# Kernel tuning notes

Hardware: AMD Instinct MI355X
Metric: run time of the kernel (lower is better)

The kernel has to match this reference:

```python
import jax, jax.numpy as jnp
import numpy as np

B, N, D_POINTS, D_MODEL = 2, 65536, 64, 128
SCALE = 1.0 / np.float32(np.sqrt(D_MODEL))


def setup_inputs() -> dict:
    key = jax.random.key(0)
    ks = jax.random.split(key, 20)
    def lin(k, fan_in, fan_out):
        s = 1.0 / np.sqrt(fan_in)
        return jax.random.uniform(k, (fan_in, fan_out), jnp.float32, -s, s)
    return {
        "xyz": jax.random.normal(ks[0], (B, N, 3), jnp.float32),
        "features": jax.random.normal(ks[1], (B, N, D_POINTS), jnp.float32),
        "fc1_w": lin(ks[2], D_POINTS, D_MODEL), "fc1_b": jnp.zeros((D_MODEL,), jnp.float32),
        "fc2_w": lin(ks[3], D_MODEL, D_POINTS), "fc2_b": jnp.zeros((D_POINTS,), jnp.float32),
        "d1_w": lin(ks[4], 3, D_MODEL), "d1_b": jnp.zeros((D_MODEL,), jnp.float32),
        "d2_w": lin(ks[5], D_MODEL, D_MODEL), "d2_b": jnp.zeros((D_MODEL,), jnp.float32),
        "g1_w": lin(ks[6], D_MODEL, D_MODEL), "g1_b": jnp.zeros((D_MODEL,), jnp.float32),
        "g2_w": lin(ks[7], D_MODEL, D_MODEL), "g2_b": jnp.zeros((D_MODEL,), jnp.float32),
        "wq": lin(ks[8], D_MODEL, D_MODEL),
        "wk": lin(ks[9], D_MODEL, D_MODEL),
        "wv": lin(ks[10], D_MODEL, D_MODEL),
    }


def reference(xyz, features, fc1_w, fc1_b, fc2_w, fc2_b, d1_w, d1_b, d2_w, d2_b,
              g1_w, g1_b, g2_w, g2_b, wq, wk, wv):
    # x: [B, N, d_model]
    x = features @ fc1_w + fc1_b
    q = x @ wq
    k = x @ wk
    v = x @ wv
    # position encoding MLP on xyz: [B, N, d_model]
    pos_enc = jax.nn.relu(xyz @ d1_w + d1_b) @ d2_w + d2_b
    # vector attention: elementwise q - k + pos_enc, gamma MLP, per-channel softmax over points
    attn = jax.nn.relu((q - k + pos_enc) @ g1_w + g1_b) @ g2_w + g2_b
    attn = jax.nn.softmax(attn * SCALE, axis=-2)  # softmax over N (point axis)
    # elementwise gating of values
    res = attn * (v + pos_enc)
    res = res @ fc2_w + fc2_b + features  # residual
    return (res, attn)
```

## Files before the change

kernel.cpp:

```cpp
#include <hip/hip_runtime.h>
#include <hip/hip_bf16.h>

#define BB 2
#define NN 65536
#define DP 64
#define DM 128
#define SCALEF 0.08838834764831845f

typedef __attribute__((ext_vector_type(8))) short short8v;
typedef __attribute__((ext_vector_type(4))) float float4v;

__device__ __forceinline__ unsigned fenc(float f) {
  unsigned u = __float_as_uint(f);
  return (u & 0x80000000u) ? ~u : (u | 0x80000000u);
}
__device__ __forceinline__ float fdec(unsigned u) {
  unsigned v = (u & 0x80000000u) ? (u & 0x7FFFFFFFu) : ~u;
  return __uint_as_float(v);
}
__device__ __forceinline__ unsigned short f2bf(float f) {
  unsigned u = __float_as_uint(f);
  u += 0x7FFFu + ((u >> 16) & 1u);
  return (unsigned short)(u >> 16);
}
__device__ __forceinline__ float bf2f(unsigned short h) {
  return __uint_as_float(((unsigned)h) << 16);
}

__global__ __launch_bounds__(256) void k0_kernel(
    const float* __restrict__ wq, const float* __restrict__ wk,
    const float* __restrict__ fc1_w, const float* __restrict__ d2_w,
    const float* __restrict__ g1_w, const float* __restrict__ g2_w,
    const float* __restrict__ wv_w,
    float* __restrict__ zbuf,
    short* __restrict__ d2t, short* __restrict__ fc1t, short* __restrict__ wqkt,
    short* __restrict__ g1t, short* __restrict__ g2t, short* __restrict__ wvt) {
  int t = threadIdx.x, bi = blockIdx.x;
  if (bi < 2) zbuf[bi * 256 + t] = 0.f;
  int mat = bi >> 5, blk = bi & 31;
  if (mat == 1) {
    int i = blk * 256 + t;
    int n = i >> 6, k = i & 63;
    fc1t[n * 64 + k] = (short)f2bf(fc1_w[k * 128 + n]);
  } else {
    const float* src = (mat == 0) ? d2_w : (mat == 2) ? wq : (mat == 3) ? g1_w
                     : (mat == 4) ? g2_w : wv_w;
    short* dst = (mat == 0) ? d2t : (mat == 2) ? wqkt : (mat == 3) ? g1t
               : (mat == 4) ? g2t : wvt;
#pragma unroll
    for (int j = 0; j < 2; ++j) {
      int i = blk * 512 + t + j * 256;
      int n = i >> 7, k = i & 127;
      float v = src[k * 128 + n];
      if (mat == 2) v -= wk[k * 128 + n];
      dst[n * 128 + k] = (short)f2bf(v);
    }
  }
}

template<int K>
__device__ __forceinline__ void gemm_mfma(const short* __restrict__ A,
                                          const short* __restrict__ Wt,
                                          short* __restrict__ Ws,
                                          int tid, int wv, int col, int quad,
                                          float4v acc[4][2]) {
#pragma unroll
  for (int h = 0; h < K / 64; ++h) {
    __syncthreads();
#pragma unroll
    for (int j = 0; j < 4; ++j) {
      int i = tid + j * 256;
      int row = i >> 3, kc = (i & 7) * 8;
      *(short8v*)(Ws + row * 72 + kc) = *(const short8v*)(Wt + row * K + h * 64 + kc);
    }
    __syncthreads();
#pragma unroll
    for (int ks = 0; ks < 2; ++ks) {
      int ko = h * 64 + ks * 32 + quad * 8;
      int wo = ks * 32 + quad * 8;
      short8v b0 = *(const short8v*)(Ws + (wv * 32 + col) * 72 + wo);
      short8v b1 = *(const short8v*)(Ws + (wv * 32 + 16 + col) * 72 + wo);
#pragma unroll
      for (int mt = 0; mt < 4; ++mt) {
        short8v a = *(const short8v*)(A + (mt * 16 + col) * 136 + ko);
        acc[mt][0] = __builtin_amdgcn_mfma_f32_16x16x32_bf16(a, b0, acc[mt][0], 0, 0, 0);
        acc[mt][1] = __builtin_amdgcn_mfma_f32_16x16x32_bf16(a, b1, acc[mt][1], 0, 0, 0);
      }
    }
  }
}

__device__ __forceinline__ void store_tile(short* __restrict__ dst,
                                           const float4v acc[4][2],
                                           int wv, int col, int quad,
                                           float b0, float b1, bool do_relu) {
#pragma unroll
  for (int mt = 0; mt < 4; ++mt)
#pragma unroll
    for (int nt = 0; nt < 2; ++nt) {
      float bias = nt ? b1 : b0;
#pragma unroll
      for (int r = 0; r < 4; ++r) {
        float v = acc[mt][nt][r] + bias;
        if (do_relu) v = fmaxf(v, 0.f);
        dst[(mt * 16 + quad * 4 + r) * 136 + wv * 32 + nt * 16 + col] = (short)f2bf(v);
      }
    }
}

__global__ __launch_bounds__(256, 2) void k1_kernel(
    const float* __restrict__ xyz, const float* __restrict__ features,
    const short* __restrict__ fc1t, const float* __restrict__ fc1_b,
    const float* __restrict__ d1_w, const float* __restrict__ d1_b,
    const short* __restrict__ d2t, const float* __restrict__ d2_b,
    const short* __restrict__ g1t, const float* __restrict__ g1_b,
    const short* __restrict__ g2t, const float* __restrict__ g2_b,
    const short* __restrict__ wqkt, const short* __restrict__ wvt,
    float* __restrict__ out_logits, unsigned short* __restrict__ Gbf,
    unsigned* __restrict__ maxenc) {
  __shared__ short As[64 * 136];
  __shared__ short Xs[64 * 136];
  __shared__ short Ws[128 * 72];

  const int tid = threadIdx.x;
  const int wv = tid >> 6;
  const int lane = tid & 63;
  const int col = lane & 15, quad = lane >> 4;
  const long long p0 = (long long)blockIdx.x * 64;
  const int b = (int)(p0 >> 16);

  float* xf = (float*)Xs;
  if (tid < 192) xf[tid] = xyz[p0 * 3 + tid];
  __syncthreads();

  {
    const int tn = tid & 31, tm = tid >> 5;
    const int c4 = tn * 4, pbase = tm * 8;
    float4 w0 = *(const float4*)(d1_w + c4);
    float4 w1 = *(const float4*)(d1_w + 128 + c4);
    float4 w2 = *(const float4*)(d1_w + 256 + c4);
    float4 bb = *(const float4*)(d1_b + c4);
#pragma unroll
    for (int p = 0; p < 8; ++p) {
      float x0 = xf[(pbase + p) * 3 + 0];
      float x1 = xf[(pbase + p) * 3 + 1];
      float x2 = xf[(pbase + p) * 3 + 2];
      short4 rr;
      rr.x = (short)f2bf(fmaxf(0.f, fmaf(x0, w0.x, fmaf(x1, w1.x, fmaf(x2, w2.x, bb.x)))));
      rr.y = (short)f2bf(fmaxf(0.f, fmaf(x0, w0.y, fmaf(x1, w1.y, fmaf(x2, w2.y, bb.y)))));
      rr.z = (short)f2bf(fmaxf(0.f, fmaf(x0, w0.z, fmaf(x1, w1.z, fmaf(x2, w2.z, bb.z)))));
      rr.w = (short)f2bf(fmaxf(0.f, fmaf(x0, w0.w, fmaf(x1, w1.w, fmaf(x2, w2.w, bb.w)))));
      *(short4*)(As + (pbase + p) * 136 + c4) = rr;
    }
  }

  const int ch0 = wv * 32 + col, ch1 = ch0 + 16;
  float4v pe[4][2], acc[4][2];

#pragma unroll
  for (int mt = 0; mt < 4; ++mt)
#pragma unroll
    for (int nt = 0; nt < 2; ++nt)
#pragma unroll
      for (int r = 0; r < 4; ++r) acc[mt][nt][r] = 0.f;
  gemm_mfma<128>(As, d2t, Ws, tid, wv, col, quad, acc);
  {
    float b0 = d2_b[ch0], b1 = d2_b[ch1];
#pragma unroll
    for (int mt = 0; mt < 4; ++mt)
#pragma unroll
      for (int r = 0; r < 4; ++r) {
        pe[mt][0][r] = acc[mt][0][r] + b0;
        pe[mt][1][r] = acc[mt][1][r] + b1;
      }
  }
  __syncthreads();

#pragma unroll
  for (int j = 0; j < 4; ++j) {
    int c = tid + j * 256;
    float4 f = *(const float4*)(features + p0 * 64 + (long long)c * 4);
    int row = c >> 4, cp = (c & 15) * 4;
    short4 s;
    s.x = (short)f2bf(f.x); s.y = (short)f2bf(f.y);
    s.z = (short)f2bf(f.z); s.w = (short)f2bf(f.w);
    *(short4*)(As + row * 136 + cp) = s;
  }
#pragma unroll
  for (int mt = 0; mt < 4; ++mt)
#pragma unroll
    for (int nt = 0; nt < 2; ++nt)
#pragma unroll
      for (int r = 0; r < 4; ++r) acc[mt][nt][r] = 0.f;
  gemm_mfma<64>(As, fc1t, Ws, tid, wv, col, quad, acc);
  store_tile(Xs, acc, wv, col, quad, fc1_b[ch0], fc1_b[ch1], false);

#pragma unroll
  for (int mt = 0; mt < 4; ++mt)
#pragma unroll
    for (int nt = 0; nt < 2; ++nt)
#pragma unroll
      for (int r = 0; r < 4; ++r) acc[mt][nt][r] = pe[mt][nt][r];
  gemm_mfma<128>(Xs, wqkt, Ws, tid, wv, col, quad, acc);
  store_tile(As, acc, wv, col, quad, 0.f, 0.f, false);

#pragma unroll
  for (int mt = 0; mt < 4; ++mt)
#pragma unroll
    for (int nt = 0; nt < 2; ++nt)
#pragma unroll
      for (int r = 0; r < 4; ++r) acc[mt][nt][r] = 0.f;
  gemm_mfma<128>(As, g1t, Ws, tid, wv, col, quad, acc);
  __syncthreads();
  store_tile(As, acc, wv, col, quad, g1_b[ch0], g1_b[ch1], true);

#pragma unroll
  for (int mt = 0; mt < 4; ++mt)
#pragma unroll
    for (int nt = 0; nt < 2; ++nt)
#pragma unroll
      for (int r = 0; r < 4; ++r) acc[mt][nt][r] = 0.f;
  gemm_mfma<128>(As, g2t, Ws, tid, wv, col, quad, acc);
  {
    float b0 = g2_b[ch0], b1 = g2_b[ch1];
    float mx0 = -3.4e38f, mx1 = -3.4e38f;
#pragma unroll
    for (int mt = 0; mt < 4; ++mt)
#pragma unroll
      for (int r = 0; r < 4; ++r) {
        long long row = p0 + mt * 16 + quad * 4 + r;
        float v0 = acc[mt][0][r] + b0;
        float v1 = acc[mt][1][r] + b1;
        out_logits[row * DM + ch0] = v0;
        out_logits[row * DM + ch1] = v1;
        mx0 = fmaxf(mx0, v0); mx1 = fmaxf(mx1, v1);
      }
    mx0 = fmaxf(mx0, __shfl_xor(mx0, 16, 64));
    mx0 = fmaxf(mx0, __shfl_xor(mx0, 32, 64));
    mx1 = fmaxf(mx1, __shfl_xor(mx1, 16, 64));
    mx1 = fmaxf(mx1, __shfl_xor(mx1, 32, 64));
    if (quad == 0) {
      atomicMax(&maxenc[b * DM + ch0], fenc(mx0));
      atomicMax(&maxenc[b * DM + ch1], fenc(mx1));
    }
  }

#pragma unroll
  for (int mt = 0; mt < 4; ++mt)
#pragma unroll
    for (int nt = 0; nt < 2; ++nt)
#pragma unroll
      for (int r = 0; r < 4; ++r) acc[mt][nt][r] = pe[mt][nt][r];
  gemm_mfma<128>(Xs, wvt, Ws, tid, wv, col, quad, acc);
#pragma unroll
  for (int mt = 0; mt < 4; ++mt)
#pragma unroll
    for (int r = 0; r < 4; ++r) {
      long long row = p0 + mt * 16 + quad * 4 + r;
      Gbf[row * DM + ch0] = f2bf(acc[mt][0][r]);
      Gbf[row * DM + ch1] = f2bf(acc[mt][1][r]);
    }
}

__global__ __launch_bounds__(256) void k2_kernel(const float* __restrict__ logits,
                                                 const unsigned* __restrict__ maxenc,
                                                 float* __restrict__ sums) {
  __shared__ float red[8 * DM];
  const int tid = threadIdx.x;
  const int c4 = (tid & 31) * 4, r = tid >> 5;
  const long long pb = (long long)blockIdx.x * 256;
  const int b = (int)(pb >> 16);
  float4 m;
  m.x = fdec(maxenc[b * DM + c4 + 0]); m.y = fdec(maxenc[b * DM + c4 + 1]);
  m.z = fdec(maxenc[b * DM + c4 + 2]); m.w = fdec(maxenc[b * DM + c4 + 3]);
  float4 s = {0.f, 0.f, 0.f, 0.f};
  for (int i = 0; i < 32; ++i) {
    long long p = pb + r + (long long)i * 8;
    float4 l = *(const float4*)(logits + p * DM + c4);
    s.x += __expf((l.x - m.x) * SCALEF);
    s.y += __expf((l.y - m.y) * SCALEF);
    s.z += __expf((l.z - m.z) * SCALEF);
    s.w += __expf((l.w - m.w) * SCALEF);
  }
  *(float4*)(red + r * DM + c4) = s;
  __syncthreads();
  if (tid < DM) {
    float t = 0.f;
#pragma unroll
    for (int rr = 0; rr < 8; ++rr) t += red[rr * DM + tid];
    atomicAdd(&sums[b * DM + tid], t);
  }
}

__global__ __launch_bounds__(256) void k3_kernel(
    float* __restrict__ attn_io,
    float* __restrict__ out_res,
    const unsigned short* __restrict__ Gbf,
    const float* __restrict__ sums, const unsigned* __restrict__ maxenc,
    const float* __restrict__ fc2_w, const float* __restrict__ fc2_b,
    const float* __restrict__ features) {
  __shared__ float Ys[64 * DM];
  __shared__ float W2[DM * DP];
  const int tid = threadIdx.x;
#pragma unroll
  for (int j = 0; j < 8; ++j)
    ((float4*)W2)[tid + j * 256] = ((const float4*)fc2_w)[tid + j * 256];

  const long long p0 = (long long)blockIdx.x * 64;
  const int b = (int)(p0 >> 16);
  const int tn = tid & 31, tm = tid >> 5;
  const int c4 = tn * 4, pbase = tm * 8;

  float4 m, sv;
  m.x = fdec(maxenc[b * DM + c4 + 0]); m.y = fdec(maxenc[b * DM + c4 + 1]);
  m.z = fdec(maxenc[b * DM + c4 + 2]); m.w = fdec(maxenc[b * DM + c4 + 3]);
  sv.x = 1.f / sums[b * DM + c4 + 0]; sv.y = 1.f / sums[b * DM + c4 + 1];
  sv.z = 1.f / sums[b * DM + c4 + 2]; sv.w = 1.f / sums[b * DM + c4 + 3];

#pragma unroll
  for (int p = 0; p < 8; ++p) {
    long long idx = (p0 + pbase + p) * DM + c4;
    float4 l = *(const float4*)(attn_io + idx);
    float4 a;
    a.x = __expf((l.x - m.x) * SCALEF) * sv.x;
    a.y = __expf((l.y - m.y) * SCALEF) * sv.y;
    a.z = __expf((l.z - m.z) * SCALEF) * sv.z;
    a.w = __expf((l.w - m.w) * SCALEF) * sv.w;
    *(float4*)(attn_io + idx) = a;
    ushort4 g = *(const ushort4*)(Gbf + idx);
    float4 y;
    y.x = a.x * bf2f(g.x); y.y = a.y * bf2f(g.y);
    y.z = a.z * bf2f(g.z); y.w = a.w * bf2f(g.w);
    *(float4*)(Ys + (pbase + p) * DM + c4) = y;
  }
  __syncthreads();

  const int tn2 = tid & 15, tm2 = tid >> 4;
  const int c4b = tn2 * 4, pb2 = tm2 * 4;
  float acc[4][4];
#pragma unroll
  for (int p = 0; p < 4; ++p)
    acc[p][0] = acc[p][1] = acc[p][2] = acc[p][3] = 0.f;

  for (int k = 0; k < DM; k += 4) {
    float4 a4[4];
#pragma unroll
    for (int p = 0; p < 4; ++p)
      a4[p] = *(const float4*)(Ys + (pb2 + p) * DM + k);
#pragma unroll
    for (int i = 0; i < 4; ++i) {
      float4 w4 = *(const float4*)(W2 + (k + i) * DP + c4b);
#pragma unroll
      for (int p = 0; p < 4; ++p) {
        float a = (i == 0) ? a4[p].x : (i == 1) ? a4[p].y : (i == 2) ? a4[p].z : a4[p].w;
        acc[p][0] = fmaf(a, w4.x, acc[p][0]);
        acc[p][1] = fmaf(a, w4.y, acc[p][1]);
        acc[p][2] = fmaf(a, w4.z, acc[p][2]);
        acc[p][3] = fmaf(a, w4.w, acc[p][3]);
      }
    }
  }
  float4 bb = *(const float4*)(fc2_b + c4b);
#pragma unroll
  for (int p = 0; p < 4; ++p) {
    float4 ft = *(const float4*)(features + (p0 + pb2 + p) * DP + c4b);
    float4 o;
    o.x = acc[p][0] + bb.x + ft.x; o.y = acc[p][1] + bb.y + ft.y;
    o.z = acc[p][2] + bb.z + ft.z; o.w = acc[p][3] + bb.w + ft.w;
    *(float4*)(out_res + (p0 + pb2 + p) * DP + c4b) = o;
  }
}

extern "C" void kernel_launch(void* const* d_in, const int* in_sizes, int n_in,
                              void* d_out, int out_size, void* d_ws, size_t ws_size,
                              hipStream_t stream) {
  const float* xyz      = (const float*)d_in[0];
  const float* features = (const float*)d_in[1];
  const float* fc1_w    = (const float*)d_in[2];
  const float* fc1_b    = (const float*)d_in[3];
  const float* fc2_w    = (const float*)d_in[4];
  const float* fc2_b    = (const float*)d_in[5];
  const float* d1_w     = (const float*)d_in[6];
  const float* d1_b     = (const float*)d_in[7];
  const float* d2_w     = (const float*)d_in[8];
  const float* d2_b     = (const float*)d_in[9];
  const float* g1_w     = (const float*)d_in[10];
  const float* g1_b     = (const float*)d_in[11];
  const float* g2_w     = (const float*)d_in[12];
  const float* g2_b     = (const float*)d_in[13];
  const float* wq       = (const float*)d_in[14];
  const float* wk       = (const float*)d_in[15];
  const float* wv       = (const float*)d_in[16];

  float* out_res  = (float*)d_out;
  float* out_attn = out_res + (long long)BB * NN * DP;

  float*    sums   = (float*)d_ws;
  unsigned* maxenc = (unsigned*)d_ws + 256;
  short* wbase = (short*)((float*)d_ws + 512);
  short* d2t  = wbase;
  short* fc1t = d2t + 16384;
  short* wqkt = fc1t + 8192;
  short* g1t  = wqkt + 16384;
  short* g2t  = g1t + 16384;
  short* wvt  = g2t + 16384;
  unsigned short* Gbf = (unsigned short*)d_out;

  hipLaunchKernelGGL(k0_kernel, dim3(192), dim3(256), 0, stream,
                     wq, wk, fc1_w, d2_w, g1_w, g2_w, wv,
                     (float*)d_ws, d2t, fc1t, wqkt, g1t, g2t, wvt);
  hipLaunchKernelGGL(k1_kernel, dim3((BB * NN) / 64), dim3(256), 0, stream,
                     xyz, features, fc1t, fc1_b, d1_w, d1_b, d2t, d2_b,
                     g1t, g1_b, g2t, g2_b, wqkt, wvt, out_attn, Gbf, maxenc);
  hipLaunchKernelGGL(k2_kernel, dim3((BB * NN) / 256), dim3(256), 0, stream,
                     out_attn, maxenc, sums);
  hipLaunchKernelGGL(k3_kernel, dim3((BB * NN) / 64), dim3(256), 0, stream,
                     out_attn, out_res, Gbf, sums, maxenc, fc2_w, fc2_b, features);
}
```

Measured before the change: 281.2 us.

## Drop max pass, fuse exp/sum into k1, MFMA fc2, register-resident weights

Removes the separate max-reduction and sum kernel. k1 now computes exp of the scaled logits directly, stores them as bf16 and atomically accumulates per-channel sums, so the softmax max subtraction is skipped. Weight tiles are loaded straight into registers instead of staged through shared memory, and occupancy is raised to three blocks. The final fc2 projection moves to bf16 MFMA with a pre-transposed weight. The risks are overflow without max subtraction if logits grow large, and extra bf16 rounding of the exponentials and of the gated values.

Result: faster. 237.1 us (-15.7%).

```diff
diff --git a/kernel.cpp b/kernel.cpp
--- a/kernel.cpp
+++ b/kernel.cpp
@@ -10,14 +10,6 @@
 typedef __attribute__((ext_vector_type(8))) short short8v;
 typedef __attribute__((ext_vector_type(4))) float float4v;
 
-__device__ __forceinline__ unsigned fenc(float f) {
-  unsigned u = __float_as_uint(f);
-  return (u & 0x80000000u) ? ~u : (u | 0x80000000u);
-}
-__device__ __forceinline__ float fdec(unsigned u) {
-  unsigned v = (u & 0x80000000u) ? (u & 0x7FFFFFFFu) : ~u;
-  return __uint_as_float(v);
-}
 __device__ __forceinline__ unsigned short f2bf(float f) {
   unsigned u = __float_as_uint(f);
   u += 0x7FFFu + ((u >> 16) & 1u);
@@ -29,19 +21,24 @@
 
 __global__ __launch_bounds__(256) void k0_kernel(
     const float* __restrict__ wq, const float* __restrict__ wk,
-    const float* __restrict__ fc1_w, const float* __restrict__ d2_w,
-    const float* __restrict__ g1_w, const float* __restrict__ g2_w,
-    const float* __restrict__ wv_w,
-    float* __restrict__ zbuf,
+    const float* __restrict__ fc1_w, const float* __restrict__ fc2_w,
+    const float* __restrict__ d2_w, const float* __restrict__ g1_w,
+    const float* __restrict__ g2_w, const float* __restrict__ wv_w,
+    float* __restrict__ sums,
     short* __restrict__ d2t, short* __restrict__ fc1t, short* __restrict__ wqkt,
-    short* __restrict__ g1t, short* __restrict__ g2t, short* __restrict__ wvt) {
+    short* __restrict__ g1t, short* __restrict__ g2t, short* __restrict__ wvt,
+    short* __restrict__ fc2t) {
   int t = threadIdx.x, bi = blockIdx.x;
-  if (bi < 2) zbuf[bi * 256 + t] = 0.f;
+  if (bi == 0) sums[t] = 0.f;
   int mat = bi >> 5, blk = bi & 31;
   if (mat == 1) {
     int i = blk * 256 + t;
     int n = i >> 6, k = i & 63;
     fc1t[n * 64 + k] = (short)f2bf(fc1_w[k * 128 + n]);
+  } else if (mat == 6) {
+    int i = blk * 256 + t;
+    int n = i >> 7, k = i & 127;
+    fc2t[n * 128 + k] = (short)f2bf(fc2_w[k * 64 + n]);
   } else {
     const float* src = (mat == 0) ? d2_w : (mat == 2) ? wq : (mat == 3) ? g1_w
                      : (mat == 4) ? g2_w : wv_w;
@@ -59,40 +56,33 @@
 }
 
 template<int K>
-__device__ __forceinline__ void gemm_mfma(const short* __restrict__ A,
-                                          const short* __restrict__ Wt,
-                                          short* __restrict__ Ws,
-                                          int tid, int wv, int col, int quad,
-                                          float4v acc[4][2]) {
-#pragma unroll
-  for (int h = 0; h < K / 64; ++h) {
-    __syncthreads();
-#pragma unroll
-    for (int j = 0; j < 4; ++j) {
-      int i = tid + j * 256;
-      int row = i >> 3, kc = (i & 7) * 8;
-      *(short8v*)(Ws + row * 72 + kc) = *(const short8v*)(Wt + row * K + h * 64 + kc);
-    }
-    __syncthreads();
-#pragma unroll
-    for (int ks = 0; ks < 2; ++ks) {
-      int ko = h * 64 + ks * 32 + quad * 8;
-      int wo = ks * 32 + quad * 8;
-      short8v b0 = *(const short8v*)(Ws + (wv * 32 + col) * 72 + wo);
-      short8v b1 = *(const short8v*)(Ws + (wv * 32 + 16 + col) * 72 + wo);
-#pragma unroll
-      for (int mt = 0; mt < 4; ++mt) {
-        short8v a = *(const short8v*)(A + (mt * 16 + col) * 136 + ko);
-        acc[mt][0] = __builtin_amdgcn_mfma_f32_16x16x32_bf16(a, b0, acc[mt][0], 0, 0, 0);
-        acc[mt][1] = __builtin_amdgcn_mfma_f32_16x16x32_bf16(a, b1, acc[mt][1], 0, 0, 0);
-      }
+__device__ __forceinline__ void loadB(const short* __restrict__ Wt,
+                                      int wid, int col, int quad, short8v b[2][4]) {
+#pragma unroll
+  for (int nt = 0; nt < 2; ++nt)
+#pragma unroll
+    for (int kt = 0; kt < K / 32; ++kt)
+      b[nt][kt] = *(const short8v*)(Wt + (wid * 32 + nt * 16 + col) * K + kt * 32 + quad * 8);
+}
+
+template<int K>
+__device__ __forceinline__ void gemm_compute(const short* __restrict__ A,
+                                             const short8v b[2][4],
+                                             int col, int quad, float4v acc[4][2]) {
+#pragma unroll
+  for (int kt = 0; kt < K / 32; ++kt) {
+#pragma unroll
+    for (int mt = 0; mt < 4; ++mt) {
+      short8v a = *(const short8v*)(A + (mt * 16 + col) * 136 + kt * 32 + quad * 8);
+      acc[mt][0] = __builtin_amdgcn_mfma_f32_16x16x32_bf16(a, b[0][kt], acc[mt][0], 0, 0, 0);
+      acc[mt][1] = __builtin_amdgcn_mfma_f32_16x16x32_bf16(a, b[1][kt], acc[mt][1], 0, 0, 0);
     }
   }
 }
 
 __device__ __forceinline__ void store_tile(short* __restrict__ dst,
                                            const float4v acc[4][2],
-                                           int wv, int col, int quad,
+                                           int wid, int col, int quad,
                                            float b0, float b1, bool do_relu) {
 #pragma unroll
   for (int mt = 0; mt < 4; ++mt)
@@ -103,12 +93,17 @@
       for (int r = 0; r < 4; ++r) {
         float v = acc[mt][nt][r] + bias;
         if (do_relu) v = fmaxf(v, 0.f);
-        dst[(mt * 16 + quad * 4 + r) * 136 + wv * 32 + nt * 16 + col] = (short)f2bf(v);
+        dst[(mt * 16 + quad * 4 + r) * 136 + wid * 32 + nt * 16 + col] = (short)f2bf(v);
       }
     }
 }
 
-__global__ __launch_bounds__(256, 2) void k1_kernel(
+#define ZERO_ACC(acc) \
+  _Pragma("unroll") for (int mt = 0; mt < 4; ++mt) \
+  _Pragma("unroll") for (int nt = 0; nt < 2; ++nt) \
+  _Pragma("unroll") for (int r = 0; r < 4; ++r) acc[mt][nt][r] = 0.f;
+
+__global__ __launch_bounds__(256, 3) void k1_kernel(
     const float* __restrict__ xyz, const float* __restrict__ features,
     const short* __restrict__ fc1t, const float* __restrict__ fc1_b,
     const float* __restrict__ d1_w, const float* __restrict__ d1_b,
@@ -116,18 +111,19 @@
     const short* __restrict__ g1t, const float* __restrict__ g1_b,
     const short* __restrict__ g2t, const float* __restrict__ g2_b,
     const short* __restrict__ wqkt, const short* __restrict__ wvt,
-    float* __restrict__ out_logits, unsigned short* __restrict__ Gbf,
-    unsigned* __restrict__ maxenc) {
-  __shared__ short As[64 * 136];
-  __shared__ short Xs[64 * 136];
-  __shared__ short Ws[128 * 72];
+    unsigned short* __restrict__ Ebf, unsigned short* __restrict__ Gbf,
+    float* __restrict__ sums) {
+  __shared__ __align__(16) short As[64 * 136];
+  __shared__ __align__(16) short Xs[64 * 136];
 
   const int tid = threadIdx.x;
-  const int wv = tid >> 6;
-  const int lane = tid & 63;
+  const int wid = tid >> 6, lane = tid & 63;
   const int col = lane & 15, quad = lane >> 4;
   const long long p0 = (long long)blockIdx.x * 64;
-  const int b = (int)(p0 >> 16);
+  const int bi = (int)(p0 >> 16);
+
+  short8v b[2][4];
+  loadB<128>(d2t, wid, col, quad, b);
 
   float* xf = (float*)Xs;
   if (tid < 192) xf[tid] = xyz[p0 * 3 + tid];
@@ -153,17 +149,13 @@
       *(short4*)(As + (pbase + p) * 136 + c4) = rr;
     }
   }
-
-  const int ch0 = wv * 32 + col, ch1 = ch0 + 16;
+  __syncthreads();
+
+  const int ch0 = wid * 32 + col, ch1 = ch0 + 16;
   float4v pe[4][2], acc[4][2];
 
-#pragma unroll
-  for (int mt = 0; mt < 4; ++mt)
-#pragma unroll
-    for (int nt = 0; nt < 2; ++nt)
-#pragma unroll
-      for (int r = 0; r < 4; ++r) acc[mt][nt][r] = 0.f;
-  gemm_mfma<128>(As, d2t, Ws, tid, wv, col, quad, acc);
+  ZERO_ACC(acc)
+  gemm_compute<128>(As, b, col, quad, acc);
   {
     float b0 = d2_b[ch0], b1 = d2_b[ch1];
 #pragma unroll
@@ -174,6 +166,7 @@
         pe[mt][1][r] = acc[mt][1][r] + b1;
       }
   }
+  loadB<64>(fc1t, wid, col, quad, b);
   __syncthreads();
 
 #pragma unroll
@@ -186,72 +179,64 @@
     s.z = (short)f2bf(f.z); s.w = (short)f2bf(f.w);
     *(short4*)(As + row * 136 + cp) = s;
   }
+  __syncthreads();
+
+  ZERO_ACC(acc)
+  gemm_compute<64>(As, b, col, quad, acc);
+  store_tile(Xs, acc, wid, col, quad, fc1_b[ch0], fc1_b[ch1], false);
+  loadB<128>(wqkt, wid, col, quad, b);
+  __syncthreads();
+
 #pragma unroll
   for (int mt = 0; mt < 4; ++mt)
 #pragma unroll
     for (int nt = 0; nt < 2; ++nt)
 #pragma unroll
-      for (int r = 0; r < 4; ++r) acc[mt][nt][r] = 0.f;
-  gemm_mfma<64>(As, fc1t, Ws, tid, wv, col, quad, acc);
-  store_tile(Xs, acc, wv, col, quad, fc1_b[ch0], fc1_b[ch1], false);
-
-#pragma unroll
-  for (int mt = 0; mt < 4; ++mt)
-#pragma unroll
-    for (int nt = 0; nt < 2; ++nt)
-#pragma unroll
       for (int r = 0; r < 4; ++r) acc[mt][nt][r] = pe[mt][nt][r];
-  gemm_mfma<128>(Xs, wqkt, Ws, tid, wv, col, quad, acc);
-  store_tile(As, acc, wv, col, quad, 0.f, 0.f, false);
-
-#pragma unroll
-  for (int mt = 0; mt < 4; ++mt)
-#pragma unroll
-    for (int nt = 0; nt < 2; ++nt)
-#pragma unroll
-      for (int r = 0; r < 4; ++r) acc[mt][nt][r] = 0.f;
-  gemm_mfma<128>(As, g1t, Ws, tid, wv, col, quad, acc);
-  __syncthreads();
-  store_tile(As, acc, wv, col, quad, g1_b[ch0], g1_b[ch1], true);
-
-#pragma unroll
-  for (int mt = 0; mt < 4; ++mt)
-#pragma unroll
-    for (int nt = 0; nt < 2; ++nt)
-#pragma unroll
-      for (int r = 0; r < 4; ++r) acc[mt][nt][r] = 0.f;
-  gemm_mfma<128>(As, g2t, Ws, tid, wv, col, quad, acc);
+  gemm_compute<128>(Xs, b, col, quad, acc);
+  store_tile(As, acc, wid, col, quad, 0.f, 0.f, false);
+  loadB<128>(g1t, wid, col, quad, b);
+  __syncthreads();
+
+  ZERO_ACC(acc)
+  gemm_compute<128>(As, b, col, quad, acc);
+  __syncthreads();
+  store_tile(As, acc, wid, col, quad, g1_b[ch0], g1_b[ch1], true);
+  loadB<128>(g2t, wid, col, quad, b);
+  __syncthreads();
+
+  ZERO_ACC(acc)
+  gemm_compute<128>(As, b, col, quad, acc);
   {
     float b0 = g2_b[ch0], b1 = g2_b[ch1];
-    float mx0 = -3.4e38f, mx1 = -3.4e38f;
+    float s0 = 0.f, s1 = 0.f;
 #pragma unroll
     for (int mt = 0; mt < 4; ++mt)
 #pragma unroll
       for (int r = 0; r < 4; ++r) {
         long long row = p0 + mt * 16 + quad * 4 + r;
-        float v0 = acc[mt][0][r] + b0;
-        float v1 = acc[mt][1][r] + b1;
-        out_logits[row * DM + ch0] = v0;
-        out_logits[row * DM + ch1] = v1;
-        mx0 = fmaxf(mx0, v0); mx1 = fmaxf(mx1, v1);
+        float e0 = __expf((acc[mt][0][r] + b0) * SCALEF);
+        float e1 = __expf((acc[mt][1][r] + b1) * SCALEF);
+        Ebf[row * DM + ch0] = f2bf(e0);
+        Ebf[row * DM + ch1] = f2bf(e1);
+        s0 += e0; s1 += e1;
       }
-    mx0 = fmaxf(mx0, __shfl_xor(mx0, 16, 64));
-    mx0 = fmaxf(mx0, __shfl_xor(mx0, 32, 64));
-    mx1 = fmaxf(mx1, __shfl_xor(mx1, 16, 64));
-    mx1 = fmaxf(mx1, __shfl_xor(mx1, 32, 64));
+    s0 += __shfl_xor(s0, 16, 64); s0 += __shfl_xor(s0, 32, 64);
+    s1 += __shfl_xor(s1, 16, 64); s1 += __shfl_xor(s1, 32, 64);
     if (quad == 0) {
-      atomicMax(&maxenc[b * DM + ch0], fenc(mx0));
-      atomicMax(&maxenc[b * DM + ch1], fenc(mx1));
-    }
-  }
-
+      atomicAdd(&sums[bi * DM + ch0], s0);
+      atomicAdd(&sums[bi * DM + ch1], s1);
+    }
+  }
+
+  loadB<128>(wvt, wid, col, quad, b);
 #pragma unroll
   for (int mt = 0; mt < 4; ++mt)
 #pragma unroll
     for (int nt = 0; nt < 2; ++nt)
 #pragma unroll
       for (int r = 0; r < 4; ++r) acc[mt][nt][r] = pe[mt][nt][r];
-  gemm_mfma<128>(Xs, wvt, Ws, tid, wv, col, quad, acc);
+  gemm_compute<128>(Xs, b, col, quad, acc);
 #pragma unroll
   for (int mt = 0; mt < 4; ++mt)
 #pragma unroll
@@ -262,113 +247,69 @@
     }
 }
 
-__global__ __launch_bounds__(256) void k2_kernel(const float* __restrict__ logits,
-                                                 const unsigned* __restrict__ maxenc,
-                                                 float* __restrict__ sums) {
-  __shared__ float red[8 * DM];
+__global__ __launch_bounds__(256) void k3_kernel(
+    const unsigned short* __restrict__ Ebf, float* __restrict__ out_attn,
+    float* __restrict__ out_res, const unsigned short* __restrict__ Gbf,
+    const float* __restrict__ sums,
+    const short* __restrict__ fc2t, const float* __restrict__ fc2_b,
+    const float* __restrict__ features) {
+  __shared__ __align__(16) short Ys[64 * 136];
   const int tid = threadIdx.x;
-  const int c4 = (tid & 31) * 4, r = tid >> 5;
-  const long long pb = (long long)blockIdx.x * 256;
-  const int b = (int)(pb >> 16);
-  float4 m;
-  m.x = fdec(maxenc[b * DM + c4 + 0]); m.y = fdec(maxenc[b * DM + c4 + 1]);
-  m.z = fdec(maxenc[b * DM + c4 + 2]); m.w = fdec(maxenc[b * DM + c4 + 3]);
-  float4 s = {0.f, 0.f, 0.f, 0.f};
-  for (int i = 0; i < 32; ++i) {
-    long long p = pb + r + (long long)i * 8;
-    float4 l = *(const float4*)(logits + p * DM + c4);
-    s.x += __expf((l.x - m.x) * SCALEF);
-    s.y += __expf((l.y - m.y) * SCALEF);
-    s.z += __expf((l.z - m.z) * SCALEF);
-    s.w += __expf((l.w - m.w) * SCALEF);
-  }
-  *(float4*)(red + r * DM + c4) = s;
-  __syncthreads();
-  if (tid < DM) {
-    float t = 0.f;
-#pragma unroll
-    for (int rr = 0; rr < 8; ++rr) t += red[rr * DM + tid];
-    atomicAdd(&sums[b * DM + tid], t);
-  }
-}
-
-__global__ __launch_bounds__(256) void k3_kernel(
-    float* __restrict__ attn_io,
-    float* __restrict__ out_res,
-    const unsigned short* __restrict__ Gbf,
-    const float* __restrict__ sums, const unsigned* __restrict__ maxenc,
-    const float* __restrict__ fc2_w, const float* __restrict__ fc2_b,
-    const float* __restrict__ features) {
-  __shared__ float Ys[64 * DM];
-  __shared__ float W2[DM * DP];
-  const int tid = threadIdx.x;
-#pragma unroll
-  for (int j = 0; j < 8; ++j)
-    ((float4*)W2)[tid + j * 256] = ((const float4*)fc2_w)[tid + j * 256];
-
   const long long p0 = (long long)blockIdx.x * 64;
-  const int b = (int)(p0 >> 16);
-  const int tn = tid & 31, tm = tid >> 5;
-  const int c4 = tn * 4, pbase = tm * 8;
-
-  float4 m, sv;
-  m.x = fdec(maxenc[b * DM + c4 + 0]); m.y = fdec(maxenc[b * DM + c4 + 1]);
-  m.z = fdec(maxenc[b * DM + c4 + 2]); m.w = fdec(maxenc[b * DM + c4 + 3]);
-  sv.x = 1.f / sums[b * DM + c4 + 0]; sv.y = 1.f / sums[b * DM + c4 + 1];
-  sv.z = 1.f / sums[b * DM + c4 + 2]; sv.w = 1.f / sums[b * DM + c4 + 3];
-
-#pragma unroll
-  for (int p = 0; p < 8; ++p) {
-    long long idx = (p0 + pbase + p) * DM + c4;
-    float4 l = *(const float4*)(attn_io + idx);
-    float4 a;
-    a.x = __expf((l.x - m.x) * SCALEF) * sv.x;
-    a.y = __expf((l.y - m.y) * SCALEF) * sv.y;
-    a.z = __expf((l.z - m.z) * SCALEF) * sv.z;
-    a.w = __expf((l.w - m.w) * SCALEF) * sv.w;
-    *(float4*)(attn_io + idx) = a;
-    ushort4 g = *(const ushort4*)(Gbf + idx);
-    float4 y;
-    y.x = a.x * bf2f(g.x); y.y = a.y * bf2f(g.y);
-    y.z = a.z * bf2f(g.z); y.w = a.w * bf2f(g.w);
-    *(float4*)(Ys + (pbase + p) * DM + c4) = y;
-  }
-  __syncthreads();
-
-  const int tn2 = tid & 15, tm2 = tid >> 4;
-  const int c4b = tn2 * 4, pb2 = tm2 * 4;
-  float acc[4][4];
-#pragma unroll
-  for (int p = 0; p < 4; ++p)
-    acc[p][0] = acc[p][1] = acc[p][2] = acc[p][3] = 0.f;
-
-  for (int k = 0; k < DM; k += 4) {
-    float4 a4[4];
-#pragma unroll
-    for (int p = 0; p < 4; ++p)
-      a4[p] = *(const float4*)(Ys + (pb2 + p) * DM + k);
-#pragma unroll
-    for (int i = 0; i < 4; ++i) {
-      float4 w4 = *(const float4*)(W2 + (k + i) * DP + c4b);
-#pragma unroll
-      for (int p = 0; p < 4; ++p) {
-        float a = (i == 0) ? a4[p].x : (i == 1) ? a4[p].y : (i == 2) ? a4[p].z : a4[p].w;
-        acc[p][0] = fmaf(a, w4.x, acc[p][0]);
-        acc[p][1] = fmaf(a, w4.y, acc[p][1]);
-        acc[p][2] = fmaf(a, w4.z, acc[p][2]);
-        acc[p][3] = fmaf(a, w4.w, acc[p][3]);
-      }
-    }
-  }
-  float4 bb = *(const float4*)(fc2_b + c4b);
-#pragma unroll
-  for (int p = 0; p < 4; ++p) {
-    float4 ft = *(const float4*)(features + (p0 + pb2 + p) * DP + c4b);
-    float4 o;
-    o.x = acc[p][0] + bb.x + ft.x; o.y = acc[p][1] + bb.y + ft.y;
-    o.z = acc[p][2] + bb.z + ft.z; o.w = acc[p][3] + bb.w + ft.w;
-    *(float4*)(out_res + (p0 + pb2 + p) * DP + c4b) = o;
-  }
+  const int bi = (int)(p0 >> 16);
+
+  {
+    const int tn = tid & 31, tm = tid >> 5;
+    const int c4 = tn * 4;
+    float4 sv = *(const float4*)(sums + bi * DM + c4);
+    float4 rs;
+    rs.x = 1.f / sv.x; rs.y = 1.f / sv.y; rs.z = 1.f / sv.z; rs.w = 1.f / sv.w;
+#pragma unroll
+    for (int pr = 0; pr < 8; ++pr) {
+      int p = tm * 8 + pr;
+      long long idx = (p0 + p) * DM + c4;
+      ushort4 e = *(const ushort4*)(Ebf + idx);
+      float4 a;
+      a.x = bf2f(e.x) * rs.x; a.y = bf2f(e.y) * rs.y;
+      a.z = bf2f(e.z) * rs.z; a.w = bf2f(e.w) * rs.w;
+      *(float4*)(out_attn + idx) = a;
+      ushort4 g = *(const ushort4*)(Gbf + idx);
+      short4 y;
+      y.x = (short)f2bf(a.x * bf2f(g.x)); y.y = (short)f2bf(a.y * bf2f(g.y));
+      y.z = (short)f2bf(a.z * bf2f(g.z)); y.w = (short)f2bf(a.w * bf2f(g.w));
+      *(short4*)(Ys + p * 136 + c4) = y;
+    }
+  }
+
+  const int wid = tid >> 6, lane = tid & 63;
+  const int col = lane & 15, quad = lane >> 4;
+  const int n = wid * 16 + col;
+  short8v bw[4];
+#pragma unroll
+  for (int kt = 0; kt < 4; ++kt)
+    bw[kt] = *(const short8v*)(fc2t + n * DM + kt * 32 + quad * 8);
+  __syncthreads();
+
+  float4v acc[4];
+#pragma unroll
+  for (int mt = 0; mt < 4; ++mt)
+#pragma unroll
+    for (int r = 0; r < 4; ++r) acc[mt][r] = 0.f;
+#pragma unroll
+  for (int kt = 0; kt < 4; ++kt)
+#pragma unroll
+    for (int mt = 0; mt < 4; ++mt) {
+      short8v a = *(const short8v*)(Ys + (mt * 16 + col) * 136 + kt * 32 + quad * 8);
+      acc[mt] = __builtin_amdgcn_mfma_f32_16x16x32_bf16(a, bw[kt], acc[mt], 0, 0, 0);
+    }
+  float bb = fc2_b[n];
+#pragma unroll
+  for (int mt = 0; mt < 4; ++mt)
+#pragma unroll
+    for (int r = 0; r < 4; ++r) {
+      long long row = p0 + mt * 16 + quad * 4 + r;
+      out_res[row * DP + n] = acc[mt][r] + bb + features[row * DP + n];
+    }
 }
 
 extern "C" void kernel_launch(void* const* d_in, const int* in_sizes, int n_in,
@@ -395,25 +336,23 @@
   float* out_res  = (float*)d_out;
   float* out_attn = out_res + (long long)BB * NN * DP;
 
-  float*    sums   = (float*)d_ws;
-  unsigned* maxenc = (unsigned*)d_ws + 256;
-  short* wbase = (short*)((float*)d_ws + 512);
-  short* d2t  = wbase;
+  float* sums = (float*)d_ws;
+  short* d2t  = (short*)(sums + 256);
   short* fc1t = d2t + 16384;
   short* wqkt = fc1t + 8192;
   short* g1t  = wqkt + 16384;
   short* g2t  = g1t + 16384;
   short* wvt  = g2t + 16384;
+  short* fc2t = wvt + 16384;
+  unsigned short* Ebf = (unsigned short*)(fc2t + 8192);
   unsigned short* Gbf = (unsigned short*)d_out;
 
-  hipLaunchKernelGGL(k0_kernel, dim3(192), dim3(256), 0, stream,
-                     wq, wk, fc1_w, d2_w, g1_w, g2_w, wv,
-                     (float*)d_ws, d2t, fc1t, wqkt, g1t, g2t, wvt);
+  hipLaunchKernelGGL(k0_kernel, dim3(224), dim3(256), 0, stream,
+                     wq, wk, fc1_w, fc2_w, d2_w, g1_w, g2_w, wv,
+                     sums, d2t, fc1t, wqkt, g1t, g2t, wvt, fc2t);
   hipLaunchKernelGGL(k1_kernel, dim3((BB * NN) / 64), dim3(256), 0, stream,
                      xyz, features, fc1t, fc1_b, d1_w, d1_b, d2t, d2_b,
-                     g1t, g1_b, g2t, g2_b, wqkt, wvt, out_attn, Gbf, maxenc);
-  hipLaunchKernelGGL(k2_kernel, dim3((BB * NN) / 256), dim3(256), 0, stream,
-                     out_attn, maxenc, sums);
+                     g1t, g1_b, g2t, g2_b, wqkt, wvt, Ebf, Gbf, sums);
   hipLaunchKernelGGL(k3_kernel, dim3((BB * NN) / 64), dim3(256), 0, stream,
-                     out_attn, out_res, Gbf, sums, maxenc, fc2_w, fc2_b, features);
-}
+                     Ebf, out_attn, out_res, Gbf, sums, fc2t, fc2_b, features);
+}
```
